# Kernel tuning notes

Hardware: AMD Instinct MI355X
Metric: run time of the kernel (lower is better)

The kernel has to match this reference:

```python
import jax, jax.numpy as jnp
import numpy as np

C_ATOM = 128
N_HEADS = 4
HEAD_DIM = C_ATOM // N_HEADS


def setup_inputs() -> dict:
    key = jax.random.key(0)
    ks = jax.random.split(key, 11)
    B, L, A = 16, 4096, 4
    x = jax.random.normal(ks[0], (B, L, A, C_ATOM), dtype=jnp.float32)
    mask = jax.random.randint(ks[1], (B, L, A), 0, 2) > 0
    mask = mask.at[..., 0].set(True)  # ensure >=1 valid atom per residue (avoids all--inf softmax)
    s = 1.0 / np.sqrt(C_ATOM)
    def lin(k):
        kw, kb = jax.random.split(k)
        W = jax.random.uniform(kw, (C_ATOM, C_ATOM), jnp.float32, -s, s)
        b = jax.random.uniform(kb, (C_ATOM,), jnp.float32, -s, s)
        return W, b
    Wq, bq = lin(ks[2])
    Wk, bk = lin(ks[3])
    Wv, bv = lin(ks[4])
    Wo, bo = lin(ks[5])
    return {"x": x, "mask": mask, "Wq": Wq, "bq": bq, "Wk": Wk, "bk": bk,
            "Wv": Wv, "bv": bv, "Wo": Wo, "bo": bo}


def reference(x, mask, Wq, bq, Wk, bk, Wv, bv, Wo, bo):
    B, L, A, C = x.shape
    H, D = N_HEADS, HEAD_DIM
    # q/k/v projections (torch Linear: x @ W.T + b)
    q = (x @ Wq.T + bq).reshape(B, L, A, H, D)
    k = (x @ Wk.T + bk).reshape(B, L, A, H, D)
    v = (x @ Wv.T + bv).reshape(B, L, A, H, D)
    scale = 1.0 / jnp.sqrt(jnp.asarray(D, x.dtype))
    # per-residue 4x4 attention scores: [B, L, H, q_atom, k_atom]
    scores = jnp.einsum("blqhd,blkhd->blhqk", q, k) * scale
    # key-side mask bias (broadcast over heads and query atoms)
    bias = jnp.where(mask[:, :, None, None, :], 0.0, -jnp.inf).astype(x.dtype)
    attn = jax.nn.softmax(scores + bias, axis=-1)
    out = jnp.einsum("blhqk,blkhd->blqhd", attn, v).reshape(B, L, A, C)
    out = out @ Wo.T + bo
    residue_mask = jnp.any(mask, axis=-1)[..., None, None].astype(out.dtype)  # [B,L,1,1]
    return out * residue_mask
```

## Files before the change

### kernel.cpp

```cpp
#include <hip/hip_runtime.h>
#include <stdint.h>


typedef __bf16 bf16x8 __attribute__((ext_vector_type(8)));
typedef float  f32x4  __attribute__((ext_vector_type(4)));

#define N_RES 65536
#define RPB   16
#define MROWS 64
#define CDIM  128

__device__ __forceinline__ uint32_t pk2(float a, float b) {
    uint32_t ua = __builtin_bit_cast(uint32_t, a) + 0x8000u;
    uint32_t ub = __builtin_bit_cast(uint32_t, b) + 0x8000u;
    return (ua >> 16) | (ub & 0xffff0000u);
}
__device__ __forceinline__ uint16_t f2bf(float a) {
    uint32_t u = __builtin_bit_cast(uint32_t, a);
    return (uint16_t)((u + 0x7fffu + ((u >> 16) & 1u)) >> 16);
}
__device__ __forceinline__ bf16x8 pack8(float4 f0, float4 f1) {
    uint4 uu = make_uint4(pk2(f0.x, f0.y), pk2(f0.z, f0.w),
                          pk2(f1.x, f1.y), pk2(f1.z, f1.w));
    return __builtin_bit_cast(bf16x8, uu);
}
__device__ __forceinline__ void bf8_unpack(uint4 u, float* f) {
    f[0] = __builtin_bit_cast(float, u.x << 16);
    f[1] = __builtin_bit_cast(float, u.x & 0xffff0000u);
    f[2] = __builtin_bit_cast(float, u.y << 16);
    f[3] = __builtin_bit_cast(float, u.y & 0xffff0000u);
    f[4] = __builtin_bit_cast(float, u.z << 16);
    f[5] = __builtin_bit_cast(float, u.z & 0xffff0000u);
    f[6] = __builtin_bit_cast(float, u.w << 16);
    f[7] = __builtin_bit_cast(float, u.w & 0xffff0000u);
}

__global__ void wconv_kernel(const float* __restrict__ wq, const float* __restrict__ wk,
                             const float* __restrict__ wv, const float* __restrict__ wo,
                             uint16_t* __restrict__ dst) {
    int i = blockIdx.x * 256 + threadIdx.x;
    const float* s = (i < 16384) ? wq : (i < 32768) ? wk : (i < 49152) ? wv : wo;
    dst[i] = f2bf(s[i & 16383]);
}

template <bool USEWS>
__global__ __launch_bounds__(256, 2)
void laa_main(const float* __restrict__ x, const int* __restrict__ mask,
              const float* __restrict__ Wq, const float* __restrict__ bq,
              const float* __restrict__ Wk, const float* __restrict__ bk,
              const float* __restrict__ Wv, const float* __restrict__ bv,
              const float* __restrict__ Wo, const float* __restrict__ bo,
              const uint16_t* __restrict__ wbf,
              float* __restrict__ out) {
    __shared__ uint16_t sQ[MROWS * CDIM];
    __shared__ uint16_t sK[MROWS * CDIM];
    __shared__ uint16_t sV[MROWS * CDIM];
    __shared__ uint16_t sO[MROWS * CDIM];

    const int tid  = threadIdx.x;
    const int wave = tid >> 6;
    const int lane = tid & 63;
    const int lrow = lane & 15;
    const int quad = lane >> 4;
    const long m0  = (long)blockIdx.x * MROWS;

    const f32x4 vzero = {0.f, 0.f, 0.f, 0.f};

    bf16x8 af[4][4];
    {
        const float* xb = x + m0 * CDIM;
        #pragma unroll
        for (int m = 0; m < 4; ++m) {
            const float* rowp = xb + (m * 16 + lrow) * CDIM;
            #pragma unroll
            for (int ks = 0; ks < 4; ++ks) {
                const float4* p = (const float4*)(rowp + ks * 32 + quad * 8);
                af[m][ks] = pack8(p[0], p[1]);
            }
        }
    }

    f32x4 acc[3][4][2];
    #pragma unroll
    for (int g = 0; g < 3; ++g)
        #pragma unroll
        for (int m = 0; m < 4; ++m)
            #pragma unroll
            for (int nt = 0; nt < 2; ++nt) acc[g][m][nt] = vzero;

    const float* wsrc32[3] = {Wq, Wk, Wv};
    #pragma unroll
    for (int ks = 0; ks < 4; ++ks) {
        bf16x8 bfr[3][2];
        #pragma unroll
        for (int g = 0; g < 3; ++g) {
            #pragma unroll
            for (int nt = 0; nt < 2; ++nt) {
                int wrow = wave * 32 + nt * 16 + lrow;
                if constexpr (USEWS) {
                    bfr[g][nt] = *(const bf16x8*)(wbf + g * 16384 + wrow * CDIM + ks * 32 + quad * 8);
                } else {
                    const float* wp = wsrc32[g] + wrow * CDIM + ks * 32 + quad * 8;
                    bfr[g][nt] = pack8(((const float4*)wp)[0], ((const float4*)wp)[1]);
                }
            }
        }
        #pragma unroll
        for (int g = 0; g < 3; ++g)
            #pragma unroll
            for (int m = 0; m < 4; ++m)
                #pragma unroll
                for (int nt = 0; nt < 2; ++nt)
                    acc[g][m][nt] = __builtin_amdgcn_mfma_f32_16x16x32_bf16(
                        af[m][ks], bfr[g][nt], acc[g][m][nt], 0, 0, 0);
    }

    {
        uint16_t* sdst[3] = {sQ, sK, sV};
        const float* bias[3] = {bq, bk, bv};
        #pragma unroll
        for (int g = 0; g < 3; ++g) {
            #pragma unroll
            for (int nt = 0; nt < 2; ++nt) {
                int col = wave * 32 + nt * 16 + lrow;
                float bb = bias[g][col];
                #pragma unroll
                for (int m = 0; m < 4; ++m) {
                    #pragma unroll
                    for (int r = 0; r < 4; ++r) {
                        int row = m * 16 + quad * 4 + r;
                        sdst[g][row * CDIM + col] = f2bf(acc[g][m][nt][r] + bb);
                    }
                }
            }
        }
    }
    __syncthreads();

    {
        const int rl = tid >> 4;
        const int h  = (tid >> 2) & 3;
        const int qa = tid & 3;
        const int rowq = rl * 4 + qa;
        const int cb = h * 32;

        const int4 mk = *(const int4*)(mask + ((long)blockIdx.x * RPB + rl) * 4);
        const int mka[4] = {mk.x, mk.y, mk.z, mk.w};

        float qv[32];
        {
            const uint4* qp = (const uint4*)(sQ + rowq * CDIM + cb);
            #pragma unroll
            for (int c = 0; c < 4; ++c) bf8_unpack(qp[c], qv + c * 8);
        }
        float sc[4];
        #pragma unroll
        for (int ka = 0; ka < 4; ++ka) {
            const uint4* kp = (const uint4*)(sK + (rl * 4 + ka) * CDIM + cb);
            float d = 0.f;
            #pragma unroll
            for (int c = 0; c < 4; ++c) {
                float kv[8]; bf8_unpack(kp[c], kv);
                #pragma unroll
                for (int j = 0; j < 8; ++j) d += qv[c * 8 + j] * kv[j];
            }
            sc[ka] = d * 0.17677669529663689f;
        }
        float mx = -3e38f;
        #pragma unroll
        for (int ka = 0; ka < 4; ++ka) if (mka[ka]) mx = fmaxf(mx, sc[ka]);
        float e[4], ssum = 0.f;
        #pragma unroll
        for (int ka = 0; ka < 4; ++ka) {
            e[ka] = mka[ka] ? __expf(sc[ka] - mx) : 0.f;
            ssum += e[ka];
        }
        const float inv = ssum > 0.f ? 1.f / ssum : 0.f;

        float o[32];
        #pragma unroll
        for (int j = 0; j < 32; ++j) o[j] = 0.f;
        #pragma unroll
        for (int ka = 0; ka < 4; ++ka) {
            float wgt = e[ka] * inv;
            const uint4* vp = (const uint4*)(sV + (rl * 4 + ka) * CDIM + cb);
            #pragma unroll
            for (int c = 0; c < 4; ++c) {
                float vv[8]; bf8_unpack(vp[c], vv);
                #pragma unroll
                for (int j = 0; j < 8; ++j) o[c * 8 + j] += wgt * vv[j];
            }
        }
        uint32_t* op = (uint32_t*)(sO + rowq * CDIM + cb);
        #pragma unroll
        for (int c2 = 0; c2 < 16; ++c2) op[c2] = pk2(o[2 * c2], o[2 * c2 + 1]);
    }
    __syncthreads();

    f32x4 acc2[4][2];
    #pragma unroll
    for (int m = 0; m < 4; ++m)
        #pragma unroll
        for (int nt = 0; nt < 2; ++nt) acc2[m][nt] = vzero;

    #pragma unroll
    for (int ks = 0; ks < 4; ++ks) {
        bf16x8 a2[4];
        #pragma unroll
        for (int m = 0; m < 4; ++m)
            a2[m] = *(const bf16x8*)(sO + (m * 16 + lrow) * CDIM + ks * 32 + quad * 8);
        bf16x8 b2[2];
        #pragma unroll
        for (int nt = 0; nt < 2; ++nt) {
            int wrow = wave * 32 + nt * 16 + lrow;
            if constexpr (USEWS) {
                b2[nt] = *(const bf16x8*)(wbf + 3 * 16384 + wrow * CDIM + ks * 32 + quad * 8);
            } else {
                const float* wp = Wo + wrow * CDIM + ks * 32 + quad * 8;
                b2[nt] = pack8(((const float4*)wp)[0], ((const float4*)wp)[1]);
            }
        }
        #pragma unroll
        for (int m = 0; m < 4; ++m)
            #pragma unroll
            for (int nt = 0; nt < 2; ++nt)
                acc2[m][nt] = __builtin_amdgcn_mfma_f32_16x16x32_bf16(
                    a2[m], b2[nt], acc2[m][nt], 0, 0, 0);
    }
    {
        #pragma unroll
        for (int m = 0; m < 4; ++m) {
            const int4 mk2 = *(const int4*)(mask + ((long)blockIdx.x * RPB + m * 4 + quad) * 4);
            const float rm = (mk2.x | mk2.y | mk2.z | mk2.w) ? 1.f : 0.f;
            #pragma unroll
            for (int nt = 0; nt < 2; ++nt) {
                int col = wave * 32 + nt * 16 + lrow;
                float bb = bo[col];
                #pragma unroll
                for (int r = 0; r < 4; ++r) {
                    long row = m0 + m * 16 + quad * 4 + r;
                    out[row * CDIM + col] = (acc2[m][nt][r] + bb) * rm;
                }
            }
        }
    }
}

extern "C" void kernel_launch(void* const* d_in, const int* in_sizes, int n_in,
                              void* d_out, int out_size, void* d_ws, size_t ws_size,
                              hipStream_t stream) {
    const float* x    = (const float*)d_in[0];
    const int*   mask = (const int*)d_in[1];
    const float* Wq   = (const float*)d_in[2];
    const float* bq   = (const float*)d_in[3];
    const float* Wk   = (const float*)d_in[4];
    const float* bk   = (const float*)d_in[5];
    const float* Wv   = (const float*)d_in[6];
    const float* bv   = (const float*)d_in[7];
    const float* Wo   = (const float*)d_in[8];
    const float* bo   = (const float*)d_in[9];
    float* out = (float*)d_out;

    const int nblocks = N_RES / RPB;
    const bool usews = ws_size >= (size_t)(4 * 16384 * sizeof(uint16_t));
    if (usews) {
        uint16_t* wbf = (uint16_t*)d_ws;
        wconv_kernel<<<256, 256, 0, stream>>>(Wq, Wk, Wv, Wo, wbf);
        laa_main<true><<<nblocks, 256, 0, stream>>>(x, mask, Wq, bq, Wk, bk, Wv, bv,
                                                    Wo, bo, wbf, out);
    } else {
        laa_main<false><<<nblocks, 256, 0, stream>>>(x, mask, Wq, bq, Wk, bk, Wv, bv,
                                                     Wo, bo, nullptr, out);
    }
}
```

Before: 331.2 us.

## Compute per-residue attention directly from MFMA accumulators, dropping Q/K/V shared staging

```diff
diff --git a/kernel.cpp b/kernel.cpp
--- a/kernel.cpp
+++ b/kernel.cpp
@@ -15,36 +15,33 @@
     uint32_t ub = __builtin_bit_cast(uint32_t, b) + 0x8000u;
     return (ua >> 16) | (ub & 0xffff0000u);
 }
-__device__ __forceinline__ uint16_t f2bf(float a) {
-    uint32_t u = __builtin_bit_cast(uint32_t, a);
-    return (uint16_t)((u + 0x7fffu + ((u >> 16) & 1u)) >> 16);
+__device__ __forceinline__ uint16_t bf1(float a) {
+    return (uint16_t)((__builtin_bit_cast(uint32_t, a) + 0x8000u) >> 16);
 }
 __device__ __forceinline__ bf16x8 pack8(float4 f0, float4 f1) {
     uint4 uu = make_uint4(pk2(f0.x, f0.y), pk2(f0.z, f0.w),
                           pk2(f1.x, f1.y), pk2(f1.z, f1.w));
     return __builtin_bit_cast(bf16x8, uu);
 }
-__device__ __forceinline__ void bf8_unpack(uint4 u, float* f) {
-    f[0] = __builtin_bit_cast(float, u.x << 16);
-    f[1] = __builtin_bit_cast(float, u.x & 0xffff0000u);
-    f[2] = __builtin_bit_cast(float, u.y << 16);
-    f[3] = __builtin_bit_cast(float, u.y & 0xffff0000u);
-    f[4] = __builtin_bit_cast(float, u.z << 16);
-    f[5] = __builtin_bit_cast(float, u.z & 0xffff0000u);
-    f[6] = __builtin_bit_cast(float, u.w << 16);
-    f[7] = __builtin_bit_cast(float, u.w & 0xffff0000u);
+__device__ __forceinline__ int swz_key(int row4) {
+    return ((row4 & 2) << 2) | ((row4 & 8) >> 1) | ((row4 & 4) >> 1) | (row4 & 1);
 }
 
 __global__ void wconv_kernel(const float* __restrict__ wq, const float* __restrict__ wk,
                              const float* __restrict__ wv, const float* __restrict__ wo,
                              uint16_t* __restrict__ dst) {
-    int i = blockIdx.x * 256 + threadIdx.x;
-    const float* s = (i < 16384) ? wq : (i < 32768) ? wk : (i < 49152) ? wv : wo;
-    dst[i] = f2bf(s[i & 16383]);
+    int gid = blockIdx.x * 256 + threadIdx.x;
+    int idx = gid * 4;
+    int sel = idx >> 14;
+    int off = idx & 16383;
+    const float* s = (sel == 0) ? wq : (sel == 1) ? wk : (sel == 2) ? wv : wo;
+    float4 f = *(const float4*)(s + off);
+    uint2 u = make_uint2(pk2(f.x, f.y), pk2(f.z, f.w));
+    *(uint2*)(dst + idx) = u;
 }
 
 template <bool USEWS>
-__global__ __launch_bounds__(256, 2)
+__global__ __launch_bounds__(256, 3)
 void laa_main(const float* __restrict__ x, const int* __restrict__ mask,
               const float* __restrict__ Wq, const float* __restrict__ bq,
               const float* __restrict__ Wk, const float* __restrict__ bk,
@@ -52,9 +49,6 @@
               const float* __restrict__ Wo, const float* __restrict__ bo,
               const uint16_t* __restrict__ wbf,
               float* __restrict__ out) {
-    __shared__ uint16_t sQ[MROWS * CDIM];
-    __shared__ uint16_t sK[MROWS * CDIM];
-    __shared__ uint16_t sV[MROWS * CDIM];
     __shared__ uint16_t sO[MROWS * CDIM];
 
     const int tid  = threadIdx.x;
@@ -65,32 +59,30 @@
     const long m0  = (long)blockIdx.x * MROWS;
 
     const f32x4 vzero = {0.f, 0.f, 0.f, 0.f};
-
-    bf16x8 af[4][4];
-    {
-        const float* xb = x + m0 * CDIM;
+    const float SC = 0.17677669529663689f;
+
+    const int c0 = wave * 32 + lrow, c1 = c0 + 16;
+    const float bq0 = bq[c0], bq1 = bq[c1];
+    const float bk0 = bk[c0], bk1 = bk[c1];
+    const float bv0 = bv[c0], bv1 = bv[c1];
+
+    f32x4 acc[3][4][2];
+    #pragma unroll
+    for (int g = 0; g < 3; ++g)
+        #pragma unroll
+        for (int m = 0; m < 4; ++m)
+            #pragma unroll
+            for (int nt = 0; nt < 2; ++nt) acc[g][m][nt] = vzero;
+
+    const float* wsrc32[3] = {Wq, Wk, Wv};
+    #pragma unroll
+    for (int ks = 0; ks < 4; ++ks) {
+        bf16x8 af[4];
         #pragma unroll
         for (int m = 0; m < 4; ++m) {
-            const float* rowp = xb + (m * 16 + lrow) * CDIM;
-            #pragma unroll
-            for (int ks = 0; ks < 4; ++ks) {
-                const float4* p = (const float4*)(rowp + ks * 32 + quad * 8);
-                af[m][ks] = pack8(p[0], p[1]);
-            }
-        }
-    }
-
-    f32x4 acc[3][4][2];
-    #pragma unroll
-    for (int g = 0; g < 3; ++g)
-        #pragma unroll
-        for (int m = 0; m < 4; ++m)
-            #pragma unroll
-            for (int nt = 0; nt < 2; ++nt) acc[g][m][nt] = vzero;
-
-    const float* wsrc32[3] = {Wq, Wk, Wv};
-    #pragma unroll
-    for (int ks = 0; ks < 4; ++ks) {
+            const float4* p = (const float4*)(x + (m0 + m * 16 + lrow) * CDIM + ks * 32 + quad * 8);
+            af[m] = pack8(p[0], p[1]);
+        }
         bf16x8 bfr[3][2];
         #pragma unroll
         for (int g = 0; g < 3; ++g) {
@@ -112,103 +104,89 @@
                 #pragma unroll
                 for (int nt = 0; nt < 2; ++nt)
                     acc[g][m][nt] = __builtin_amdgcn_mfma_f32_16x16x32_bf16(
-                        af[m][ks], bfr[g][nt], acc[g][m][nt], 0, 0, 0);
-    }
-
-    {
-        uint16_t* sdst[3] = {sQ, sK, sV};
-        const float* bias[3] = {bq, bk, bv};
-        #pragma unroll
-        for (int g = 0; g < 3; ++g) {
+                        af[m], bfr[g][nt], acc[g][m][nt], 0, 0, 0);
+    }
+
+    const int key_w = swz_key(quad * 4);
+    #pragma unroll
+    for (int m = 0; m < 4; ++m) {
+        const int4 mk = *(const int4*)(mask + ((long)blockIdx.x * RPB + m * 4 + quad) * 4);
+        const int mka[4] = {mk.x, mk.y, mk.z, mk.w};
+
+        float qv[4][2], kv[4][2], vv[4][2];
+        #pragma unroll
+        for (int r = 0; r < 4; ++r) {
+            qv[r][0] = (acc[0][m][0][r] + bq0) * SC;
+            qv[r][1] = (acc[0][m][1][r] + bq1) * SC;
+            kv[r][0] =  acc[1][m][0][r] + bk0;
+            kv[r][1] =  acc[1][m][1][r] + bk1;
+            vv[r][0] =  acc[2][m][0][r] + bv0;
+            vv[r][1] =  acc[2][m][1][r] + bv1;
+        }
+        float t[16];
+        #pragma unroll
+        for (int qa = 0; qa < 4; ++qa)
+            #pragma unroll
+            for (int ka = 0; ka < 4; ++ka)
+                t[qa * 4 + ka] = qv[qa][0] * kv[ka][0] + qv[qa][1] * kv[ka][1];
+        #pragma unroll
+        for (int s = 1; s < 16; s <<= 1)
+            #pragma unroll
+            for (int i = 0; i < 16; ++i)
+                t[i] += __shfl_xor(t[i], s, 16);
+
+        float o[4][2];
+        #pragma unroll
+        for (int qa = 0; qa < 4; ++qa) {
+            float mx = -3.0e38f;
+            #pragma unroll
+            for (int ka = 0; ka < 4; ++ka)
+                mx = mka[ka] ? fmaxf(mx, t[qa * 4 + ka]) : mx;
+            float e[4], ssum = 0.f;
+            #pragma unroll
+            for (int ka = 0; ka < 4; ++ka) {
+                e[ka] = mka[ka] ? __expf(t[qa * 4 + ka] - mx) : 0.f;
+                ssum += e[ka];
+            }
+            const float inv = ssum > 0.f ? 1.f / ssum : 0.f;
+            float o0 = 0.f, o1 = 0.f;
+            #pragma unroll
+            for (int ka = 0; ka < 4; ++ka) {
+                float w = e[ka] * inv;
+                o0 += w * vv[ka][0];
+                o1 += w * vv[ka][1];
+            }
+            o[qa][0] = o0; o[qa][1] = o1;
+        }
+        #pragma unroll
+        for (int r = 0; r < 4; ++r) {
+            const int row = m * 16 + quad * 4 + r;
+            const int key = key_w ^ swz_key(r);
             #pragma unroll
             for (int nt = 0; nt < 2; ++nt) {
-                int col = wave * 32 + nt * 16 + lrow;
-                float bb = bias[g][col];
-                #pragma unroll
-                for (int m = 0; m < 4; ++m) {
-                    #pragma unroll
-                    for (int r = 0; r < 4; ++r) {
-                        int row = m * 16 + quad * 4 + r;
-                        sdst[g][row * CDIM + col] = f2bf(acc[g][m][nt][r] + bb);
-                    }
-                }
+                const int col = wave * 32 + nt * 16 + lrow;
+                const int c8 = col >> 3, j = col & 7;
+                sO[row * CDIM + ((c8 ^ key) << 3) + j] = bf1(o[r][nt]);
             }
         }
     }
     __syncthreads();
 
-    {
-        const int rl = tid >> 4;
-        const int h  = (tid >> 2) & 3;
-        const int qa = tid & 3;
-        const int rowq = rl * 4 + qa;
-        const int cb = h * 32;
-
-        const int4 mk = *(const int4*)(mask + ((long)blockIdx.x * RPB + rl) * 4);
-        const int mka[4] = {mk.x, mk.y, mk.z, mk.w};
-
-        float qv[32];
-        {
-            const uint4* qp = (const uint4*)(sQ + rowq * CDIM + cb);
-            #pragma unroll
-            for (int c = 0; c < 4; ++c) bf8_unpack(qp[c], qv + c * 8);
-        }
-        float sc[4];
-        #pragma unroll
-        for (int ka = 0; ka < 4; ++ka) {
-            const uint4* kp = (const uint4*)(sK + (rl * 4 + ka) * CDIM + cb);
-            float d = 0.f;
-            #pragma unroll
-            for (int c = 0; c < 4; ++c) {
-                float kv[8]; bf8_unpack(kp[c], kv);
-                #pragma unroll
-                for (int j = 0; j < 8; ++j) d += qv[c * 8 + j] * kv[j];
-            }
-            sc[ka] = d * 0.17677669529663689f;
-        }
-        float mx = -3e38f;
-        #pragma unroll
-        for (int ka = 0; ka < 4; ++ka) if (mka[ka]) mx = fmaxf(mx, sc[ka]);
-        float e[4], ssum = 0.f;
-        #pragma unroll
-        for (int ka = 0; ka < 4; ++ka) {
-            e[ka] = mka[ka] ? __expf(sc[ka] - mx) : 0.f;
-            ssum += e[ka];
-        }
-        const float inv = ssum > 0.f ? 1.f / ssum : 0.f;
-
-        float o[32];
-        #pragma unroll
-        for (int j = 0; j < 32; ++j) o[j] = 0.f;
-        #pragma unroll
-        for (int ka = 0; ka < 4; ++ka) {
-            float wgt = e[ka] * inv;
-            const uint4* vp = (const uint4*)(sV + (rl * 4 + ka) * CDIM + cb);
-            #pragma unroll
-            for (int c = 0; c < 4; ++c) {
-                float vv[8]; bf8_unpack(vp[c], vv);
-                #pragma unroll
-                for (int j = 0; j < 8; ++j) o[c * 8 + j] += wgt * vv[j];
-            }
-        }
-        uint32_t* op = (uint32_t*)(sO + rowq * CDIM + cb);
-        #pragma unroll
-        for (int c2 = 0; c2 < 16; ++c2) op[c2] = pk2(o[2 * c2], o[2 * c2 + 1]);
-    }
-    __syncthreads();
-
     f32x4 acc2[4][2];
     #pragma unroll
     for (int m = 0; m < 4; ++m)
         #pragma unroll
         for (int nt = 0; nt < 2; ++nt) acc2[m][nt] = vzero;
 
+    const int key_r = swz_key(lrow);
     #pragma unroll
     for (int ks = 0; ks < 4; ++ks) {
         bf16x8 a2[4];
         #pragma unroll
-        for (int m = 0; m < 4; ++m)
-            a2[m] = *(const bf16x8*)(sO + (m * 16 + lrow) * CDIM + ks * 32 + quad * 8);
+        for (int m = 0; m < 4; ++m) {
+            const int c8 = ks * 4 + quad;
+            a2[m] = *(const bf16x8*)(sO + (m * 16 + lrow) * CDIM + ((c8 ^ key_r) << 3));
+        }
         bf16x8 b2[2];
         #pragma unroll
         for (int nt = 0; nt < 2; ++nt) {
@@ -265,7 +243,7 @@
     const bool usews = ws_size >= (size_t)(4 * 16384 * sizeof(uint16_t));
     if (usews) {
         uint16_t* wbf = (uint16_t*)d_ws;
-        wconv_kernel<<<256, 256, 0, stream>>>(Wq, Wk, Wv, Wo, wbf);
+        wconv_kernel<<<64, 256, 0, stream>>>(Wq, Wk, Wv, Wo, wbf);
         laa_main<true><<<nblocks, 256, 0, stream>>>(x, mask, Wq, bq, Wk, bk, Wv, bv,
                                                     Wo, bo, wbf, out);
     } else {
```

Result: slower. 353.3 us (+6.7%).
